# Performance work log

Measured on AMD Instinct MI355X. Metric: run time of the kernel, lower is better.

## Reference

```python
import jax, jax.numpy as jnp
import numpy as np

N_NODES, N_EDGES, N_FEAT = 50000, 500000, 128
HID, LAT, N_GRAPHS = 256, 64, 512
HEADS, DH = 8, 32  # GAT: 8 heads x 32 = 256
EPS = 1e-5


def _seg_softmax(logits, seg, num):
    m = jax.ops.segment_max(logits, seg, num_segments=num)
    m = jnp.where(jnp.isfinite(m), m, 0.0)
    e = jnp.exp(logits - m[seg])
    s = jax.ops.segment_sum(e, seg, num_segments=num)
    return e / jnp.maximum(s[seg], 1e-16)


def _bn(h, g, b):  # BatchNorm1d, batch statistics
    mu = h.mean(0)
    var = h.var(0)
    return (h - mu) * jax.lax.rsqrt(var + EPS) * g + b


def _ln(h, g, b):
    mu = h.mean(-1, keepdims=True)
    var = h.var(-1, keepdims=True)
    return (h - mu) * jax.lax.rsqrt(var + EPS) * g + b


def setup_inputs() -> dict:
    key = jax.random.key(0)
    ks = iter(jax.random.split(key, 40))
    f = lambda *s: jax.random.normal(next(ks), s, dtype=jnp.float32) * 0.05
    inp = {
        'x': jax.random.normal(next(ks), (N_NODES, N_FEAT), dtype=jnp.float32),
        'W_emb': f(N_FEAT, HID), 'b_emb': f(HID),
        'W_gcn': f(HID, HID), 'b_gcn': f(HID),
        'W_gat': f(HID, HID), 'a_src': f(HEADS, DH), 'a_dst': f(HEADS, DH), 'b_gat': f(HID),
        'W_l': f(HID, HID), 'b_l': f(HID), 'W_r': f(HID, HID),
        'bn_gamma': jnp.ones((3, HID), jnp.float32), 'bn_beta': jnp.zeros((3, HID), jnp.float32),
        'Wg1': f(HID, HID // 2), 'bg1': f(HID // 2), 'Wg2': f(HID // 2, 1), 'bg2': f(1),
        'Wm1': f(HID, HID), 'bm1': f(HID), 'ln_m_g': jnp.ones(HID, jnp.float32), 'ln_m_b': jnp.zeros(HID, jnp.float32),
        'Wm2': f(HID, LAT), 'bm2': f(LAT),
        'Wv1': f(HID, HID), 'bv1': f(HID), 'ln_v_g': jnp.ones(HID, jnp.float32), 'ln_v_b': jnp.zeros(HID, jnp.float32),
        'Wv2': f(HID, LAT), 'bv2': f(LAT),
        'edge_index': jax.random.randint(next(ks), (2, N_EDGES), 0, N_NODES, dtype=jnp.int64),
        'batch': jnp.sort(jax.random.randint(next(ks), (N_NODES,), 0, N_GRAPHS, dtype=jnp.int64)),
    }
    return inp


def _forward(x, W_emb, b_emb, W_gcn, b_gcn, W_gat, a_src, a_dst, b_gat,
             W_l, b_l, W_r, bn_gamma, bn_beta, Wg1, bg1, Wg2, bg2,
             Wm1, bm1, ln_m_g, ln_m_b, Wm2, bm2, Wv1, bv1, ln_v_g, ln_v_b, Wv2, bv2,
             edge_index, batch):
    N = x.shape[0]
    loops = jnp.arange(N)
    src_sl = jnp.concatenate([edge_index[0], loops])  # with self-loops (GCN/GAT)
    dst_sl = jnp.concatenate([edge_index[1], loops])

    h = x @ W_emb + b_emb  # [N, HID]

    # --- layer 0: GCNConv ---
    deg = jax.ops.segment_sum(jnp.ones_like(dst_sl, dtype=h.dtype), dst_sl, num_segments=N)
    dis = jax.lax.rsqrt(deg)
    norm = dis[src_sl] * dis[dst_sl]  # [E+N]
    xt = h @ W_gcn
    out = jax.ops.segment_sum(xt[src_sl] * norm[:, None], dst_sl, num_segments=N) + b_gcn
    out = jax.nn.relu(_bn(out, bn_gamma[0], bn_beta[0]))
    h = h + out

    # --- layer 1: GATConv (8 heads, concat) ---
    xt = (h @ W_gat).reshape(N, HEADS, DH)
    al_src = (xt * a_src).sum(-1)  # [N, H]
    al_dst = (xt * a_dst).sum(-1)
    logits = jax.nn.leaky_relu(al_src[src_sl] + al_dst[dst_sl], 0.2)  # [E+N, H]
    alpha = _seg_softmax(logits, dst_sl, N)
    out = jax.ops.segment_sum(xt[src_sl] * alpha[:, :, None], dst_sl, num_segments=N)
    out = out.reshape(N, HID) + b_gat
    out = jax.nn.relu(_bn(out, bn_gamma[1], bn_beta[1]))
    h = h + out

    # --- layer 2: SAGEConv (mean aggregation, no self-loops) ---
    src, dst = edge_index[0], edge_index[1]
    cnt = jax.ops.segment_sum(jnp.ones_like(dst, dtype=h.dtype), dst, num_segments=N)
    nb_mean = jax.ops.segment_sum(h[src], dst, num_segments=N) / jnp.maximum(cnt, 1.0)[:, None]
    out = nb_mean @ W_l + b_l + h @ W_r
    out = jax.nn.relu(_bn(out, bn_gamma[2], bn_beta[2]))
    h = h + out

    # --- GlobalAttention pooling ---
    gate = (jax.nn.relu(h @ Wg1 + bg1) @ Wg2 + bg2)[:, 0]  # [N]
    w = _seg_softmax(gate, batch, N_GRAPHS)
    h_graph = jax.ops.segment_sum(h * w[:, None], batch, num_segments=N_GRAPHS)  # [G, HID]

    mu = jax.nn.relu(_ln(h_graph @ Wm1 + bm1, ln_m_g, ln_m_b)) @ Wm2 + bm2
    logvar = jax.nn.relu(_ln(h_graph @ Wv1 + bv1, ln_v_g, ln_v_b)) @ Wv2 + bv2
    return mu, logvar


def reference(x, W_emb, b_emb, W_gcn, b_gcn, W_gat, a_src, a_dst, b_gat,
              W_l, b_l, W_r, bn_gamma, bn_beta, Wg1, bg1, Wg2, bg2,
              Wm1, bm1, ln_m_g, ln_m_b, Wm2, bm2, Wv1, bv1, ln_v_g, ln_v_b, Wv2, bv2,
              edge_index, batch):
    return _forward(x, W_emb, b_emb, W_gcn, b_gcn, W_gat, a_src, a_dst, b_gat,
                    W_l, b_l, W_r, bn_gamma, bn_beta, Wg1, bg1, Wg2, bg2,
                    Wm1, bm1, ln_m_g, ln_m_b, Wm2, bm2, Wv1, bv1, ln_v_g, ln_v_b, Wv2, bv2,
                    edge_index, batch)
```

## Files before the change

kernel.cpp:

```cpp
#include <hip/hip_runtime.h>
#include <cstdint>
#include <cstddef>

#define N_NODES 50000
#define N_EDGES 500000
#define NG 512
#define HID 256
#define EPS 1e-5f
#define SCB 49

typedef __attribute__((ext_vector_type(8))) __bf16 bf16x8;
typedef __attribute__((ext_vector_type(8))) ushort u16x8;
typedef __attribute__((ext_vector_type(4))) float f32x4;

__device__ __forceinline__ ushort f2bf(float f) {
  uint32_t u = __float_as_uint(f);
  uint32_t r = (u + 0x7fffu + ((u >> 16) & 1u)) >> 16;
  return (ushort)r;
}
__device__ __forceinline__ float bfu(ushort u) { return __uint_as_float(((uint32_t)u) << 16); }
__device__ __forceinline__ float4 bf4(ushort4 u) {
  return make_float4(bfu(u.x), bfu(u.y), bfu(u.z), bfu(u.w));
}

__global__ void k_csr_count(const int* __restrict__ ei, int* __restrict__ cnt) {
  int e = blockIdx.x * 256 + threadIdx.x;
  if (e < N_EDGES) atomicAdd(&cnt[ei[N_EDGES + e]], 1);
}

__global__ void k_scan_part(const int* __restrict__ cnt, int* __restrict__ psum) {
  __shared__ int red[256];
  int tid = threadIdx.x;
  int i0 = blockIdx.x * 1024 + tid * 4;
  int s = 0;
  if (i0 + 4 <= N_NODES) {
    int4 v = *reinterpret_cast<const int4*>(cnt + i0);
    s = v.x + v.y + v.z + v.w;
  } else {
    for (int k = 0; k < 4; k++)
      if (i0 + k < N_NODES) s += cnt[i0 + k];
  }
  red[tid] = s;
  __syncthreads();
  for (int o = 128; o > 0; o >>= 1) {
    if (tid < o) red[tid] += red[tid + o];
    __syncthreads();
  }
  if (tid == 0) psum[blockIdx.x] = red[0];
}

__global__ void k_scan_top(const int* __restrict__ psum, int* __restrict__ boff,
                           int* __restrict__ row_ptr) {
  int t = threadIdx.x;
  int v = (t < SCB) ? psum[t] : 0;
  int own = v;
  for (int o = 1; o < 64; o <<= 1) {
    int u = __shfl_up(v, o);
    if (t >= o) v += u;
  }
  if (t < SCB) boff[t] = v - own;
  if (t == 63) row_ptr[N_NODES] = v;
}

__global__ void k_scan_out(const int* __restrict__ cnt, const int* __restrict__ boff,
                           int* __restrict__ row_ptr, float* __restrict__ dis) {
  __shared__ int ps[256];
  int tid = threadIdx.x;
  int i0 = blockIdx.x * 1024 + tid * 4;
  int v[4];
#pragma unroll
  for (int k = 0; k < 4; k++) v[k] = (i0 + k < N_NODES) ? cnt[i0 + k] : 0;
  int s = v[0] + v[1] + v[2] + v[3];
  ps[tid] = s;
  __syncthreads();
  for (int o = 1; o < 256; o <<= 1) {
    int add = (tid >= o) ? ps[tid - o] : 0;
    __syncthreads();
    ps[tid] += add;
    __syncthreads();
  }
  int run = boff[blockIdx.x] + ((tid > 0) ? ps[tid - 1] : 0);
#pragma unroll
  for (int k = 0; k < 4; k++) {
    if (i0 + k < N_NODES) {
      row_ptr[i0 + k] = run;
      dis[i0 + k] = rsqrtf((float)v[k] + 1.0f);
      run += v[k];
    }
  }
}

__global__ void k_csr_fill(const int* __restrict__ ei, const int* __restrict__ row_ptr,
                           int* __restrict__ fill, int* __restrict__ col_src) {
  int e = blockIdx.x * 256 + threadIdx.x;
  if (e >= N_EDGES) return;
  int s = ei[e], d = ei[N_EDGES + e];
  int pos = row_ptr[d] + atomicAdd(&fill[d], 1);
  col_src[pos] = s;
}

struct WtArgs {
  const float* src[6];
  ushort* dst[6];
  int K[6];
  int C[6];
  int off[6];
};

__global__ void k_wt_all(WtArgs a) {
  int b = blockIdx.x;
  int ji = 0;
#pragma unroll
  for (int t = 1; t < 6; t++)
    if (b >= a.off[t]) ji = t;
  int K = a.K[ji], C = a.C[ji];
  int i = (b - a.off[ji]) * 256 + threadIdx.x;
  int c = i / K, k = i - c * K;
  a.dst[ji][i] = f2bf(a.src[ji][k * C + c]);
}

template <int K, int C, bool DUAL, bool AFP32, bool GATE, bool GATAL>
__global__ __launch_bounds__(512) void k_mgemm(
    const void* __restrict__ A1v, const ushort* __restrict__ W1t,
    const ushort* __restrict__ A2, const ushort* __restrict__ W2t,
    const float* __restrict__ bias, ushort* __restrict__ out_bf,
    const float* __restrict__ gw, const float* __restrict__ gb,
    float* __restrict__ gate, const float* __restrict__ asv,
    const float* __restrict__ adv, float* __restrict__ als,
    float* __restrict__ ald, int M, int relu) {
  constexpr int KS = K / 32;
  constexpr int CHK = K / 8;
  constexpr int NPAN = C / 64;
  constexpr int NISS = (64 * CHK) / 512;
  constexpr int NTOT = NPAN * (DUAL ? 2 : 1);
  constexpr int PELEM = 64 * K;
  __shared__ ushort wlds[2 * PELEM];
  const int tid = threadIdx.x;
  const int lane = tid & 63;
  const int wid = tid >> 6;
  const int r16 = lane & 15;
  const int kg = lane >> 4;
  const int rbase = blockIdx.x * 128 + wid * 16;

  int arow = rbase + r16;
  if (arow >= M) arow = M - 1;

  bf16x8 af[KS], af2[KS];
  if constexpr (AFP32) {
    const float* ap = (const float*)A1v + (size_t)arow * K + kg * 8;
#pragma unroll
    for (int ks = 0; ks < KS; ks++) {
      float4 lo = *reinterpret_cast<const float4*>(ap + ks * 32);
      float4 hi = *reinterpret_cast<const float4*>(ap + ks * 32 + 4);
      union { u16x8 u; bf16x8 b; } cv;
      cv.u = (u16x8){f2bf(lo.x), f2bf(lo.y), f2bf(lo.z), f2bf(lo.w),
                     f2bf(hi.x), f2bf(hi.y), f2bf(hi.z), f2bf(hi.w)};
      af[ks] = cv.b;
    }
  } else {
    const ushort* ap = (const ushort*)A1v + (size_t)arow * K + kg * 8;
#pragma unroll
    for (int ks = 0; ks < KS; ks++)
      af[ks] = *reinterpret_cast<const bf16x8*>(ap + ks * 32);
  }
  if constexpr (DUAL) {
    const ushort* ap = A2 + (size_t)arow * K + kg * 8;
#pragma unroll
    for (int ks = 0; ks < KS; ks++)
      af2[ks] = *reinterpret_cast<const bf16x8*>(ap + ks * 32);
  }

  float greg[4] = {0.f, 0.f, 0.f, 0.f};
  f32x4 acc[4];

#define STAGE_ASYNC(WSRC, PAN, BUF)                                            \
  {                                                                            \
    const ushort* base_ = (WSRC) + (size_t)((PAN) * 64) * K;                   \
    _Pragma("unroll") for (int j = 0; j < NISS; j++) {                         \
      int p_ = j * 512 + tid;                                                  \
      int c_ = p_ / CHK, jj_ = p_ % CHK;                                       \
      const ushort* g_ = base_ + c_ * K + (jj_ ^ (c_ & 7)) * 8;                \
      ushort* l_ = &wlds[(BUF) * PELEM + (j * 512 + wid * 64) * 8];            \
      __builtin_amdgcn_global_load_lds(                                        \
          (const __attribute__((address_space(1))) void*)(g_),                 \
          (__attribute__((address_space(3))) void*)(l_), 16, 0, 0);            \
    }                                                                          \
  }

#define COMPUTE(AF, BUF)                                                       \
  {                                                                            \
    const ushort* wb_ = &wlds[(BUF) * PELEM];                                  \
    _Pragma("unroll") for (int ct = 0; ct < 4; ct++) {                         \
      bf16x8 wf[KS];                                                           \
      int colr = ct * 16 + r16;                                                \
      _Pragma("unroll") for (int ks = 0; ks < KS; ks++) {                      \
        int slot = colr * CHK + ((ks * 4 + kg) ^ (r16 & 7));                   \
        wf[ks] = *reinterpret_cast<const bf16x8*>(&wb_[slot * 8]);             \
      }                                                                        \
      _Pragma("unroll") for (int ks = 0; ks < KS; ks++)                        \
        acc[ct] = __builtin_amdgcn_mfma_f32_16x16x32_bf16((AF)[ks], wf[ks],    \
                                                          acc[ct], 0, 0, 0);   \
    }                                                                          \
  }

  STAGE_ASYNC(W1t, 0, 0);
  __syncthreads();

#pragma unroll
  for (int q = 0; q < NTOT; q++) {
    const int pan = DUAL ? (q >> 1) : q;
    const int pass = DUAL ? (q & 1) : 0;
    const int cur = q & 1;
    const int c0 = pan * 64;
    if (pass == 0) {
#pragma unroll
      for (int ct = 0; ct < 4; ct++) acc[ct] = (f32x4){0.f, 0.f, 0.f, 0.f};
    }
    if (q + 1 < NTOT) {
      const int npan = DUAL ? ((q + 1) >> 1) : (q + 1);
      const ushort* Wq = (DUAL && ((q + 1) & 1)) ? W2t : W1t;
      STAGE_ASYNC(Wq, npan, cur ^ 1);
    }
    if (DUAL && pass) {
      COMPUTE(af2, cur);
    } else {
      COMPUTE(af, cur);
    }
    if (pass == (DUAL ? 1 : 0)) {
      if constexpr (GATE) {
#pragma unroll
        for (int ct = 0; ct < 4; ct++) {
          int col = c0 + ct * 16 + r16;
          float bv = bias[col];
          float wv = gw[col];
#pragma unroll
          for (int i = 0; i < 4; i++) {
            float v = fmaxf(acc[ct][i] + bv, 0.f);
            greg[i] = fmaf(v, wv, greg[i]);
          }
        }
      } else {
#pragma unroll
        for (int ct = 0; ct < 4; ct++) {
          int col = c0 + ct * 16 + r16;
          float bv = bias ? bias[col] : 0.f;
#pragma unroll
          for (int i = 0; i < 4; i++) {
            int row = rbase + kg * 4 + i;
            if (row < M) {
              float v = acc[ct][i] + bv;
              if (relu) v = fmaxf(v, 0.f);
              out_bf[(size_t)row * C + col] = f2bf(v);
            }
          }
        }
      }
      if constexpr (GATAL) {
        float ps_[2][4], pd_[2][4];
#pragma unroll
        for (int h2 = 0; h2 < 2; h2++)
#pragma unroll
          for (int i = 0; i < 4; i++) { ps_[h2][i] = 0.f; pd_[h2][i] = 0.f; }
#pragma unroll
        for (int ct = 0; ct < 4; ct++) {
          int col = c0 + ct * 16 + r16;
          float as_ = asv[col], ad_ = adv[col];
          int h2 = ct >> 1;
#pragma unroll
          for (int i = 0; i < 4; i++) {
            ps_[h2][i] = fmaf(acc[ct][i], as_, ps_[h2][i]);
            pd_[h2][i] = fmaf(acc[ct][i], ad_, pd_[h2][i]);
          }
        }
#pragma unroll
        for (int h2 = 0; h2 < 2; h2++)
#pragma unroll
          for (int i = 0; i < 4; i++) {
#pragma unroll
            for (int o = 1; o < 16; o <<= 1) {
              ps_[h2][i] += __shfl_xor(ps_[h2][i], o);
              pd_[h2][i] += __shfl_xor(pd_[h2][i], o);
            }
          }
        if (r16 == 0) {
#pragma unroll
          for (int i = 0; i < 4; i++) {
            int row = rbase + kg * 4 + i;
            if (row < M) {
              als[row * 8 + pan * 2 + 0] = ps_[0][i];
              ald[row * 8 + pan * 2 + 0] = pd_[0][i];
              als[row * 8 + pan * 2 + 1] = ps_[1][i];
              ald[row * 8 + pan * 2 + 1] = pd_[1][i];
            }
          }
        }
      }
    }
    __syncthreads();
  }

  if constexpr (GATE) {
#pragma unroll
    for (int i = 0; i < 4; i++) {
#pragma unroll
      for (int o = 1; o < 16; o <<= 1) greg[i] += __shfl_xor(greg[i], o);
    }
    if (r16 == 0) {
      float b0 = gb[0];
#pragma unroll
      for (int i = 0; i < 4; i++) {
        int row = rbase + kg * 4 + i;
        if (row < M) gate[row] = greg[i] + b0;
      }
    }
  }
#undef STAGE_ASYNC
#undef COMPUTE
}

__global__ void k_gcn_agg(const ushort* __restrict__ xt, const float* __restrict__ dis,
                          const int* __restrict__ row_ptr, const int* __restrict__ col_src,
                          const float* __restrict__ b_gcn, ushort* __restrict__ outb) {
  int node = blockIdx.x * 4 + (threadIdx.x >> 6);
  if (node >= N_NODES) return;
  int lane = threadIdx.x & 63;
  int half = lane >> 5;
  int c0 = (lane & 31) * 8;
  float di = dis[node];
  float acc[8];
#pragma unroll
  for (int j = 0; j < 8; j++) acc[j] = 0.f;
  int b = row_ptr[node], e = row_ptr[node + 1];
  int g0 = b;
  for (; g0 + 8 <= e; g0 += 8) {
    int i0 = g0 + half * 4;
    int s0 = col_src[i0], s1 = col_src[i0 + 1], s2 = col_src[i0 + 2], s3 = col_src[i0 + 3];
    float w0 = di * dis[s0], w1 = di * dis[s1], w2 = di * dis[s2], w3 = di * dis[s3];
    u16x8 u0 = *reinterpret_cast<const u16x8*>(xt + (size_t)s0 * HID + c0);
    u16x8 u1 = *reinterpret_cast<const u16x8*>(xt + (size_t)s1 * HID + c0);
    u16x8 u2 = *reinterpret_cast<const u16x8*>(xt + (size_t)s2 * HID + c0);
    u16x8 u3 = *reinterpret_cast<const u16x8*>(xt + (size_t)s3 * HID + c0);
#pragma unroll
    for (int j = 0; j < 8; j++) {
      acc[j] = fmaf(bfu(u0[j]), w0, acc[j]);
      acc[j] = fmaf(bfu(u1[j]), w1, acc[j]);
      acc[j] = fmaf(bfu(u2[j]), w2, acc[j]);
      acc[j] = fmaf(bfu(u3[j]), w3, acc[j]);
    }
  }
  for (; g0 + 4 <= e; g0 += 4) {
    int i0 = g0 + half * 2;
    int s0 = col_src[i0], s1 = col_src[i0 + 1];
    float w0 = di * dis[s0], w1 = di * dis[s1];
    u16x8 u0 = *reinterpret_cast<const u16x8*>(xt + (size_t)s0 * HID + c0);
    u16x8 u1 = *reinterpret_cast<const u16x8*>(xt + (size_t)s1 * HID + c0);
#pragma unroll
    for (int j = 0; j < 8; j++) {
      acc[j] = fmaf(bfu(u0[j]), w0, acc[j]);
      acc[j] = fmaf(bfu(u1[j]), w1, acc[j]);
    }
  }
  {
    int i0 = g0 + half * 2;
    int s0 = 0, s1 = 0;
    float w0 = 0.f, w1 = 0.f;
    if (i0 < e) { s0 = col_src[i0]; w0 = di * dis[s0]; }
    if (i0 + 1 < e) { s1 = col_src[i0 + 1]; w1 = di * dis[s1]; }
    u16x8 u0 = *reinterpret_cast<const u16x8*>(xt + (size_t)s0 * HID + c0);
    u16x8 u1 = *reinterpret_cast<const u16x8*>(xt + (size_t)s1 * HID + c0);
#pragma unroll
    for (int j = 0; j < 8; j++) {
      acc[j] = fmaf(bfu(u0[j]), w0, acc[j]);
      acc[j] = fmaf(bfu(u1[j]), w1, acc[j]);
    }
  }
#pragma unroll
  for (int j = 0; j < 8; j++) acc[j] += __shfl_xor(acc[j], 32);
  if (!half) {
    u16x8 un = *reinterpret_cast<const u16x8*>(xt + (size_t)node * HID + c0);
    float w0 = di * di;
    u16x8 r;
#pragma unroll
    for (int j = 0; j < 8; j++) {
      float v = fmaf(bfu(un[j]), w0, acc[j]) + b_gcn[c0 + j];
      r[j] = f2bf(v);
    }
    *reinterpret_cast<u16x8*>(outb + (size_t)node * HID + c0) = r;
  }
}

__device__ __forceinline__ float leaky02(float x) { return x > 0.f ? x : 0.2f * x; }

__global__ void k_gat_agg(const ushort* __restrict__ xt, const float* __restrict__ alsrc,
                          const float* __restrict__ aldst, const int* __restrict__ row_ptr,
                          const int* __restrict__ col_src, const float* __restrict__ b_gat,
                          ushort* __restrict__ outb) {
  int node = blockIdx.x * 4 + (threadIdx.x >> 6);
  if (node >= N_NODES) return;
  int lane = threadIdx.x & 63;
  int half = lane >> 5;
  int l32 = lane & 31;
  int c0 = l32 * 8;
  int hh = l32 >> 2;
  float ad = aldst[node * 8 + hh];
  float acc[8];
#pragma unroll
  for (int j = 0; j < 8; j++) acc[j] = 0.f;
  float s = 0.f;
  int b = row_ptr[node], e = row_ptr[node + 1];
  int g0 = b;
  for (; g0 + 8 <= e; g0 += 8) {
    int i0 = g0 + half * 4;
    int s0 = col_src[i0], s1 = col_src[i0 + 1], s2 = col_src[i0 + 2], s3 = col_src[i0 + 3];
    float g0v = alsrc[s0 * 8 + hh], g1v = alsrc[s1 * 8 + hh];
    float g2v = alsrc[s2 * 8 + hh], g3v = alsrc[s3 * 8 + hh];
    u16x8 u0 = *reinterpret_cast<const u16x8*>(xt + (size_t)s0 * HID + c0);
    u16x8 u1 = *reinterpret_cast<const u16x8*>(xt + (size_t)s1 * HID + c0);
    u16x8 u2 = *reinterpret_cast<const u16x8*>(xt + (size_t)s2 * HID + c0);
    u16x8 u3 = *reinterpret_cast<const u16x8*>(xt + (size_t)s3 * HID + c0);
    float a0 = __expf(leaky02(g0v + ad));
    float a1 = __expf(leaky02(g1v + ad));
    float a2 = __expf(leaky02(g2v + ad));
    float a3 = __expf(leaky02(g3v + ad));
    s += a0 + a1 + a2 + a3;
#pragma unroll
    for (int j = 0; j < 8; j++) {
      acc[j] = fmaf(bfu(u0[j]), a0, acc[j]);
      acc[j] = fmaf(bfu(u1[j]), a1, acc[j]);
      acc[j] = fmaf(bfu(u2[j]), a2, acc[j]);
      acc[j] = fmaf(bfu(u3[j]), a3, acc[j]);
    }
  }
  for (; g0 + 4 <= e; g0 += 4) {
    int i0 = g0 + half * 2;
    int s0 = col_src[i0], s1 = col_src[i0 + 1];
    float a0 = __expf(leaky02(alsrc[s0 * 8 + hh] + ad));
    float a1 = __expf(leaky02(alsrc[s1 * 8 + hh] + ad));
    u16x8 u0 = *reinterpret_cast<const u16x8*>(xt + (size_t)s0 * HID + c0);
    u16x8 u1 = *reinterpret_cast<const u16x8*>(xt + (size_t)s1 * HID + c0);
    s += a0 + a1;
#pragma unroll
    for (int j = 0; j < 8; j++) {
      acc[j] = fmaf(bfu(u0[j]), a0, acc[j]);
      acc[j] = fmaf(bfu(u1[j]), a1, acc[j]);
    }
  }
  {
    int i0 = g0 + half * 2;
    int s0 = 0, s1 = 0;
    float a0 = 0.f, a1 = 0.f;
    if (i0 < e) { s0 = col_src[i0]; a0 = __expf(leaky02(alsrc[s0 * 8 + hh] + ad)); }
    if (i0 + 1 < e) { s1 = col_src[i0 + 1]; a1 = __expf(leaky02(alsrc[s1 * 8 + hh] + ad)); }
    u16x8 u0 = *reinterpret_cast<const u16x8*>(xt + (size_t)s0 * HID + c0);
    u16x8 u1 = *reinterpret_cast<const u16x8*>(xt + (size_t)s1 * HID + c0);
    s += a0 + a1;
#pragma unroll
    for (int j = 0; j < 8; j++) {
      acc[j] = fmaf(bfu(u0[j]), a0, acc[j]);
      acc[j] = fmaf(bfu(u1[j]), a1, acc[j]);
    }
  }
#pragma unroll
  for (int j = 0; j < 8; j++) acc[j] += __shfl_xor(acc[j], 32);
  s += __shfl_xor(s, 32);
  if (!half) {
    float e0 = __expf(leaky02(alsrc[node * 8 + hh] + ad));
    u16x8 un = *reinterpret_cast<const u16x8*>(xt + (size_t)node * HID + c0);
    float inv_s = 1.0f / (s + e0);
    u16x8 r;
#pragma unroll
    for (int j = 0; j < 8; j++) {
      float v = fmaf(bfu(un[j]), e0, acc[j]) * inv_s + b_gat[c0 + j];
      r[j] = f2bf(v);
    }
    *reinterpret_cast<u16x8*>(outb + (size_t)node * HID + c0) = r;
  }
}

__global__ void k_sage_agg(const ushort* __restrict__ h, const int* __restrict__ row_ptr,
                           const int* __restrict__ col_src, ushort* __restrict__ outb) {
  int node = blockIdx.x * 4 + (threadIdx.x >> 6);
  if (node >= N_NODES) return;
  int lane = threadIdx.x & 63;
  int half = lane >> 5;
  int c0 = (lane & 31) * 8;
  float acc[8];
#pragma unroll
  for (int j = 0; j < 8; j++) acc[j] = 0.f;
  int b = row_ptr[node], e = row_ptr[node + 1];
  int g0 = b;
  for (; g0 + 8 <= e; g0 += 8) {
    int i0 = g0 + half * 4;
    int s0 = col_src[i0], s1 = col_src[i0 + 1], s2 = col_src[i0 + 2], s3 = col_src[i0 + 3];
    u16x8 u0 = *reinterpret_cast<const u16x8*>(h + (size_t)s0 * HID + c0);
    u16x8 u1 = *reinterpret_cast<const u16x8*>(h + (size_t)s1 * HID + c0);
    u16x8 u2 = *reinterpret_cast<const u16x8*>(h + (size_t)s2 * HID + c0);
    u16x8 u3 = *reinterpret_cast<const u16x8*>(h + (size_t)s3 * HID + c0);
#pragma unroll
    for (int j = 0; j < 8; j++)
      acc[j] += (bfu(u0[j]) + bfu(u1[j])) + (bfu(u2[j]) + bfu(u3[j]));
  }
  for (; g0 + 4 <= e; g0 += 4) {
    int i0 = g0 + half * 2;
    int s0 = col_src[i0], s1 = col_src[i0 + 1];
    u16x8 u0 = *reinterpret_cast<const u16x8*>(h + (size_t)s0 * HID + c0);
    u16x8 u1 = *reinterpret_cast<const u16x8*>(h + (size_t)s1 * HID + c0);
#pragma unroll
    for (int j = 0; j < 8; j++) acc[j] += bfu(u0[j]) + bfu(u1[j]);
  }
  {
    int i0 = g0 + half * 2;
    int s0 = 0, s1 = 0;
    float w0 = 0.f, w1 = 0.f;
    if (i0 < e) { s0 = col_src[i0]; w0 = 1.f; }
    if (i0 + 1 < e) { s1 = col_src[i0 + 1]; w1 = 1.f; }
    u16x8 u0 = *reinterpret_cast<const u16x8*>(h + (size_t)s0 * HID + c0);
    u16x8 u1 = *reinterpret_cast<const u16x8*>(h + (size_t)s1 * HID + c0);
#pragma unroll
    for (int j = 0; j < 8; j++) {
      acc[j] = fmaf(bfu(u0[j]), w0, acc[j]);
      acc[j] = fmaf(bfu(u1[j]), w1, acc[j]);
    }
  }
#pragma unroll
  for (int j = 0; j < 8; j++) acc[j] += __shfl_xor(acc[j], 32);
  if (!half) {
    float inv = 1.0f / fmaxf((float)(e - b), 1.0f);
    u16x8 r;
#pragma unroll
    for (int j = 0; j < 8; j++) r[j] = f2bf(acc[j] * inv);
    *reinterpret_cast<u16x8*>(outb + (size_t)node * HID + c0) = r;
  }
}

__global__ void k_bn_stats(const ushort* __restrict__ x, float* __restrict__ stats) {
  int c = threadIdx.x;
  float s = 0.f, q = 0.f;
  for (int r = blockIdx.x; r < N_NODES; r += gridDim.x) {
    float v = bfu(x[(size_t)r * HID + c]);
    s += v;
    q = fmaf(v, v, q);
  }
  atomicAdd(&stats[c], s);
  atomicAdd(&stats[HID + c], q);
}

__global__ void k_bn_apply(const ushort* __restrict__ x, const float* __restrict__ stats,
                           const float* __restrict__ gamma, const float* __restrict__ beta,
                           ushort* __restrict__ h_bf) {
  const float invN = 1.0f / (float)N_NODES;
  int total = N_NODES * 64;
  for (int i = blockIdx.x * 256 + threadIdx.x; i < total; i += gridDim.x * 256) {
    int c4 = (i & 63) * 4;
    float4 xv = bf4(*reinterpret_cast<const ushort4*>(x + (size_t)i * 4));
    float4 sm = *reinterpret_cast<const float4*>(stats + c4);
    float4 sq = *reinterpret_cast<const float4*>(stats + HID + c4);
    float4 gm = *reinterpret_cast<const float4*>(gamma + c4);
    float4 bt = *reinterpret_cast<const float4*>(beta + c4);
    float4 hv = bf4(*reinterpret_cast<const ushort4*>(h_bf + (size_t)i * 4));
#define BN1(f)                                                    \
  {                                                               \
    float mu = sm.f * invN;                                       \
    float var = sq.f * invN - mu * mu;                            \
    float sc = gm.f * rsqrtf(var + EPS);                          \
    float v = (xv.f - mu) * sc + bt.f;                            \
    hv.f += fmaxf(v, 0.f);                                        \
  }
    BN1(x) BN1(y) BN1(z) BN1(w)
#undef BN1
    *reinterpret_cast<ushort4*>(h_bf + (size_t)i * 4) =
        make_ushort4(f2bf(hv.x), f2bf(hv.y), f2bf(hv.z), f2bf(hv.w));
  }
}

__global__ void k_gstart(const int* __restrict__ batch, int* __restrict__ gstart) {
  int g = blockIdx.x * 256 + threadIdx.x;
  if (g > NG) return;
  int lo = 0, hi = N_NODES;
  while (lo < hi) {
    int mid = (lo + hi) >> 1;
    if (batch[mid] < g) lo = mid + 1; else hi = mid;
  }
  gstart[g] = lo;
}

__global__ void k_pool(const ushort* __restrict__ hb, const float* __restrict__ gate,
                       const int* __restrict__ gstart, float* __restrict__ hg) {
  __shared__ float red[256];
  __shared__ float wbuf[256];
  int g = blockIdx.x, tid = threadIdx.x;
  int b = gstart[g], e = gstart[g + 1];
  float m = -1e30f;
  for (int r = b + tid; r < e; r += 256) m = fmaxf(m, gate[r]);
  red[tid] = m;
  __syncthreads();
  for (int o = 128; o > 0; o >>= 1) {
    if (tid < o) red[tid] = fmaxf(red[tid], red[tid + o]);
    __syncthreads();
  }
  m = red[0];
  __syncthreads();
  float s = 0.f;
  for (int r = b + tid; r < e; r += 256) s += __expf(gate[r] - m);
  red[tid] = s;
  __syncthreads();
  for (int o = 128; o > 0; o >>= 1) {
    if (tid < o) red[tid] += red[tid + o];
    __syncthreads();
  }
  float inv = 1.0f / fmaxf(red[0], 1e-16f);
  __syncthreads();
  float acc = 0.f;
  for (int cb = b; cb < e; cb += 256) {
    int r = cb + tid;
    wbuf[tid] = (r < e) ? __expf(gate[r] - m) : 0.f;
    __syncthreads();
    int n = min(256, e - cb);
    for (int j = 0; j < n; j++)
      acc = fmaf(bfu(hb[(size_t)(cb + j) * HID + tid]), wbuf[j], acc);
    __syncthreads();
  }
  hg[(size_t)g * HID + tid] = acc * inv;
}

__global__ void k_mlp(const float* __restrict__ hg, const float* __restrict__ W1,
                      const float* __restrict__ b1, const float* __restrict__ lng,
                      const float* __restrict__ lnb, const float* __restrict__ W2,
                      const float* __restrict__ b2, float* __restrict__ out) {
  __shared__ float row[HID];
  __shared__ float z[HID];
  __shared__ float red[HID];
  int g = blockIdx.x, tid = threadIdx.x;
  row[tid] = hg[(size_t)g * HID + tid];
  __syncthreads();
  float acc = b1[tid];
  for (int k = 0; k < HID; k++) acc = fmaf(row[k], W1[(size_t)k * HID + tid], acc);
  red[tid] = acc;
  __syncthreads();
  for (int o = 128; o > 0; o >>= 1) {
    if (tid < o) red[tid] += red[tid + o];
    __syncthreads();
  }
  float mu = red[0] * (1.0f / HID);
  __syncthreads();
  red[tid] = acc * acc;
  __syncthreads();
  for (int o = 128; o > 0; o >>= 1) {
    if (tid < o) red[tid] += red[tid + o];
    __syncthreads();
  }
  float var = red[0] * (1.0f / HID) - mu * mu;
  float zz = (acc - mu) * rsqrtf(var + EPS) * lng[tid] + lnb[tid];
  z[tid] = fmaxf(zz, 0.f);
  __syncthreads();
  if (tid < 64) {
    float o = b2[tid];
    for (int k = 0; k < HID; k++) o = fmaf(z[k], W2[(size_t)k * 64 + tid], o);
    out[(size_t)g * 64 + tid] = o;
  }
}

extern "C" void kernel_launch(void* const* d_in, const int* in_sizes, int n_in,
                              void* d_out, int out_size, void* d_ws, size_t ws_size,
                              hipStream_t stream) {
  const float* x     = (const float*)d_in[0];
  const float* W_emb = (const float*)d_in[1];
  const float* b_emb = (const float*)d_in[2];
  const float* W_gcn = (const float*)d_in[3];
  const float* b_gcn = (const float*)d_in[4];
  const float* W_gat = (const float*)d_in[5];
  const float* a_src = (const float*)d_in[6];
  const float* a_dst = (const float*)d_in[7];
  const float* b_gat = (const float*)d_in[8];
  const float* W_l   = (const float*)d_in[9];
  const float* b_l   = (const float*)d_in[10];
  const float* W_r   = (const float*)d_in[11];
  const float* bn_g  = (const float*)d_in[12];
  const float* bn_b  = (const float*)d_in[13];
  const float* Wg1   = (const float*)d_in[14];
  const float* bg1   = (const float*)d_in[15];
  const float* Wg2   = (const float*)d_in[16];
  const float* bg2   = (const float*)d_in[17];
  const float* Wm1   = (const float*)d_in[18];
  const float* bm1   = (const float*)d_in[19];
  const float* lnmg  = (const float*)d_in[20];
  const float* lnmb  = (const float*)d_in[21];
  const float* Wm2   = (const float*)d_in[22];
  const float* bm2   = (const float*)d_in[23];
  const float* Wv1   = (const float*)d_in[24];
  const float* bv1   = (const float*)d_in[25];
  const float* lnvg  = (const float*)d_in[26];
  const float* lnvb  = (const float*)d_in[27];
  const float* Wv2   = (const float*)d_in[28];
  const float* bv2   = (const float*)d_in[29];
  const int* ei      = (const int*)d_in[30];
  const int* batch   = (const int*)d_in[31];
  float* out = (float*)d_out;

  float* ws = (float*)d_ws;
  float* h     = ws;
  float* t1    = h + (size_t)N_NODES * HID;
  float* alsrc = t1 + (size_t)N_NODES * HID;
  float* aldst = alsrc + N_NODES * 8;
  float* dis   = aldst + N_NODES * 8;
  float* gate  = dis + N_NODES;
  float* hg    = gate + N_NODES;
  float* zbase = hg + NG * HID;
  float* bnst  = zbase;
  int* row_cnt = (int*)(zbase + 3 * 512);
  int* fill    = row_cnt + N_NODES;
  int* row_ptr = fill + N_NODES;
  int* col_src = row_ptr + N_NODES + 1;
  int* gstart  = col_src + N_EDGES;
  int* psum    = gstart + NG + 1;
  int* boff    = psum + 64;

  ushort* t1b = (ushort*)t1;

  size_t off = (size_t)((char*)(boff + 64) - (char*)d_ws);
  off = (off + 15) & ~(size_t)15;
  ushort* h_bf   = (ushort*)((char*)d_ws + off);
  ushort* t0_bf  = h_bf + (size_t)N_NODES * HID;
  ushort* wemb_t = t0_bf + (size_t)N_NODES * HID;
  ushort* wgcn_t = wemb_t + 128 * 256;
  ushort* wgat_t = wgcn_t + 256 * 256;
  ushort* wr_t   = wgat_t + 256 * 256;
  ushort* wl_t   = wr_t + 256 * 256;
  ushort* wg1_t  = wl_t + 256 * 256;

  size_t zbytes = (size_t)3 * 512 * 4 + 2 * (size_t)N_NODES * 4;
  hipMemsetAsync(zbase, 0, zbytes, stream);

  k_csr_count<<<(N_EDGES + 255) / 256, 256, 0, stream>>>(ei, row_cnt);
  k_scan_part<<<SCB, 256, 0, stream>>>(row_cnt, psum);
  k_scan_top<<<1, 64, 0, stream>>>(psum, boff, row_ptr);
  k_scan_out<<<SCB, 256, 0, stream>>>(row_cnt, boff, row_ptr, dis);
  k_csr_fill<<<(N_EDGES + 255) / 256, 256, 0, stream>>>(ei, row_ptr, fill, col_src);

  WtArgs wa;
  wa.src[0] = W_emb; wa.dst[0] = wemb_t; wa.K[0] = 128; wa.C[0] = 256; wa.off[0] = 0;
  wa.src[1] = W_gcn; wa.dst[1] = wgcn_t; wa.K[1] = 256; wa.C[1] = 256; wa.off[1] = 128;
  wa.src[2] = W_gat; wa.dst[2] = wgat_t; wa.K[2] = 256; wa.C[2] = 256; wa.off[2] = 384;
  wa.src[3] = W_r;   wa.dst[3] = wr_t;   wa.K[3] = 256; wa.C[3] = 256; wa.off[3] = 640;
  wa.src[4] = W_l;   wa.dst[4] = wl_t;   wa.K[4] = 256; wa.C[4] = 256; wa.off[4] = 896;
  wa.src[5] = Wg1;   wa.dst[5] = wg1_t;  wa.K[5] = 256; wa.C[5] = 128; wa.off[5] = 1152;
  k_wt_all<<<1280, 256, 0, stream>>>(wa);

  const int RB = (N_NODES + 127) / 128;
  const int AB = (N_NODES + 3) / 4;

  k_mgemm<128, 256, false, true, false, false><<<RB, 512, 0, stream>>>(
      x, wemb_t, nullptr, nullptr, b_emb, h_bf, nullptr, nullptr, nullptr,
      nullptr, nullptr, nullptr, nullptr, N_NODES, 0);

  k_mgemm<256, 256, false, false, false, false><<<RB, 512, 0, stream>>>(
      h_bf, wgcn_t, nullptr, nullptr, nullptr, t0_bf, nullptr, nullptr, nullptr,
      nullptr, nullptr, nullptr, nullptr, N_NODES, 0);
  k_gcn_agg<<<AB, 256, 0, stream>>>(t0_bf, dis, row_ptr, col_src, b_gcn, t1b);
  k_bn_stats<<<256, 256, 0, stream>>>(t1b, bnst);
  k_bn_apply<<<1024, 256, 0, stream>>>(t1b, bnst, bn_g, bn_b, h_bf);

  k_mgemm<256, 256, false, false, false, true><<<RB, 512, 0, stream>>>(
      h_bf, wgat_t, nullptr, nullptr, nullptr, t0_bf, nullptr, nullptr, nullptr,
      a_src, a_dst, alsrc, aldst, N_NODES, 0);
  k_gat_agg<<<AB, 256, 0, stream>>>(t0_bf, alsrc, aldst, row_ptr, col_src, b_gat, t1b);
  k_bn_stats<<<256, 256, 0, stream>>>(t1b, bnst + 512);
  k_bn_apply<<<1024, 256, 0, stream>>>(t1b, bnst + 512, bn_g + HID, bn_b + HID, h_bf);

  k_sage_agg<<<AB, 256, 0, stream>>>(h_bf, row_ptr, col_src, t0_bf);
  k_mgemm<256, 256, true, false, false, false><<<RB, 512, 0, stream>>>(
      h_bf, wr_t, t0_bf, wl_t, b_l, t1b, nullptr, nullptr, nullptr,
      nullptr, nullptr, nullptr, nullptr, N_NODES, 0);
  k_bn_stats<<<256, 256, 0, stream>>>(t1b, bnst + 1024);
  k_bn_apply<<<1024, 256, 0, stream>>>(t1b, bnst + 1024, bn_g + 2 * HID, bn_b + 2 * HID, h_bf);

  k_mgemm<256, 128, false, false, true, false><<<RB, 512, 0, stream>>>(
      h_bf, wg1_t, nullptr, nullptr, bg1, nullptr, Wg2, bg2, gate,
      nullptr, nullptr, nullptr, nullptr, N_NODES, 1);
  k_gstart<<<3, 256, 0, stream>>>(batch, gstart);
  k_pool<<<NG, 256, 0, stream>>>(h_bf, gate, gstart, hg);

  k_mlp<<<NG, 256, 0, stream>>>(hg, Wm1, bm1, lnmg, lnmb, Wm2, bm2, out);
  k_mlp<<<NG, 256, 0, stream>>>(hg, Wv1, bv1, lnvg, lnvb, Wv2, bv2, out + (size_t)NG * 64);
}
```

Measured before the change: 604.5 us.

## Fuse BatchNorm apply into following GEMM A-load and vectorize BN stats

BatchNorm statistics now use 8-wide vector loads with shared-memory reduction before the global atomics. Scale and shift are computed once per channel in a tiny coefficient kernel. For the GCN and SAGE layers, the normalize, ReLU and residual step is folded into the next GEMM's A-operand load, which also writes the updated residual back. This removes two standalone apply passes over the 50000x256 activation. The GAT layer keeps a simpler apply kernel.

Result: faster. 549.4 us (-9.1%).

```diff
diff --git a/kernel.cpp b/kernel.cpp
--- a/kernel.cpp
+++ b/kernel.cpp
@@ -119,7 +119,7 @@
   a.dst[ji][i] = f2bf(a.src[ji][k * C + c]);
 }
 
-template <int K, int C, bool DUAL, bool AFP32, bool GATE, bool GATAL>
+template <int K, int C, bool DUAL, bool AFP32, bool GATE, bool GATAL, bool BNF>
 __global__ __launch_bounds__(512) void k_mgemm(
     const void* __restrict__ A1v, const ushort* __restrict__ W1t,
     const ushort* __restrict__ A2, const ushort* __restrict__ W2t,
@@ -127,7 +127,8 @@
     const float* __restrict__ gw, const float* __restrict__ gb,
     float* __restrict__ gate, const float* __restrict__ asv,
     const float* __restrict__ adv, float* __restrict__ als,
-    float* __restrict__ ald, int M, int relu) {
+    float* __restrict__ ald, const float* __restrict__ scsh,
+    ushort* __restrict__ hbuf, int M, int relu) {
   constexpr int KS = K / 32;
   constexpr int CHK = K / 8;
   constexpr int NPAN = C / 64;
@@ -142,11 +143,36 @@
   const int kg = lane >> 4;
   const int rbase = blockIdx.x * 128 + wid * 16;
 
+  const bool avalid = (rbase + r16) < M;
   int arow = rbase + r16;
   if (arow >= M) arow = M - 1;
 
   bf16x8 af[KS], af2[KS];
-  if constexpr (AFP32) {
+  if constexpr (BNF) {
+    const ushort* xp = (const ushort*)A1v + (size_t)arow * K + kg * 8;
+    ushort* hp = hbuf + (size_t)arow * K + kg * 8;
+#pragma unroll
+    for (int ks = 0; ks < KS; ks++) {
+      int col = kg * 8 + ks * 32;
+      u16x8 xv = *reinterpret_cast<const u16x8*>(xp + ks * 32);
+      u16x8 hv = *reinterpret_cast<const u16x8*>(hp + ks * 32);
+      float4 sc0 = *reinterpret_cast<const float4*>(scsh + col);
+      float4 sc1 = *reinterpret_cast<const float4*>(scsh + col + 4);
+      float4 sh0 = *reinterpret_cast<const float4*>(scsh + 256 + col);
+      float4 sh1 = *reinterpret_cast<const float4*>(scsh + 256 + col + 4);
+      float scv[8] = {sc0.x, sc0.y, sc0.z, sc0.w, sc1.x, sc1.y, sc1.z, sc1.w};
+      float shv[8] = {sh0.x, sh0.y, sh0.z, sh0.w, sh1.x, sh1.y, sh1.z, sh1.w};
+      union { u16x8 u; bf16x8 b; } cv;
+#pragma unroll
+      for (int j = 0; j < 8; j++) {
+        float v = fmaf(bfu(xv[j]), scv[j], shv[j]);
+        float hn = bfu(hv[j]) + fmaxf(v, 0.f);
+        cv.u[j] = f2bf(hn);
+      }
+      af[ks] = cv.b;
+      if (avalid) *reinterpret_cast<u16x8*>(hp + ks * 32) = cv.u;
+    }
+  } else if constexpr (AFP32) {
     const float* ap = (const float*)A1v + (size_t)arow * K + kg * 8;
 #pragma unroll
     for (int ks = 0; ks < KS; ks++) {
@@ -533,41 +559,62 @@
   }
 }
 
-__global__ void k_bn_stats(const ushort* __restrict__ x, float* __restrict__ stats) {
+__global__ __launch_bounds__(256) void k_bn_stats(const ushort* __restrict__ x,
+                                                  float* __restrict__ stats) {
+  int tid = threadIdx.x;
+  int cg = tid & 31;
+  int rs = tid >> 5;
+  int c0 = cg * 8;
+  float s[8], q[8];
+#pragma unroll
+  for (int j = 0; j < 8; j++) { s[j] = 0.f; q[j] = 0.f; }
+  for (int r = blockIdx.x * 8 + rs; r < N_NODES; r += gridDim.x * 8) {
+    u16x8 v = *reinterpret_cast<const u16x8*>(x + (size_t)r * HID + c0);
+#pragma unroll
+    for (int j = 0; j < 8; j++) {
+      float f = bfu(v[j]);
+      s[j] += f;
+      q[j] = fmaf(f, f, q[j]);
+    }
+  }
+  __shared__ float ls[512];
+  ls[tid] = 0.f;
+  ls[tid + 256] = 0.f;
+  __syncthreads();
+#pragma unroll
+  for (int j = 0; j < 8; j++) {
+    atomicAdd(&ls[c0 + j], s[j]);
+    atomicAdd(&ls[256 + c0 + j], q[j]);
+  }
+  __syncthreads();
+  atomicAdd(&stats[tid], ls[tid]);
+  atomicAdd(&stats[tid + 256], ls[tid + 256]);
+}
+
+__global__ void k_bn_coef(const float* __restrict__ stats, const float* __restrict__ gamma,
+                          const float* __restrict__ beta, float* __restrict__ scsh) {
   int c = threadIdx.x;
-  float s = 0.f, q = 0.f;
-  for (int r = blockIdx.x; r < N_NODES; r += gridDim.x) {
-    float v = bfu(x[(size_t)r * HID + c]);
-    s += v;
-    q = fmaf(v, v, q);
-  }
-  atomicAdd(&stats[c], s);
-  atomicAdd(&stats[HID + c], q);
-}
-
-__global__ void k_bn_apply(const ushort* __restrict__ x, const float* __restrict__ stats,
-                           const float* __restrict__ gamma, const float* __restrict__ beta,
+  const float invN = 1.0f / (float)N_NODES;
+  float mu = stats[c] * invN;
+  float var = stats[256 + c] * invN - mu * mu;
+  float sc = gamma[c] * rsqrtf(var + EPS);
+  scsh[c] = sc;
+  scsh[256 + c] = beta[c] - mu * sc;
+}
+
+__global__ void k_bn_apply(const ushort* __restrict__ x, const float* __restrict__ scsh,
                            ushort* __restrict__ h_bf) {
-  const float invN = 1.0f / (float)N_NODES;
   int total = N_NODES * 64;
   for (int i = blockIdx.x * 256 + threadIdx.x; i < total; i += gridDim.x * 256) {
     int c4 = (i & 63) * 4;
     float4 xv = bf4(*reinterpret_cast<const ushort4*>(x + (size_t)i * 4));
-    float4 sm = *reinterpret_cast<const float4*>(stats + c4);
-    float4 sq = *reinterpret_cast<const float4*>(stats + HID + c4);
-    float4 gm = *reinterpret_cast<const float4*>(gamma + c4);
-    float4 bt = *reinterpret_cast<const float4*>(beta + c4);
+    float4 sc = *reinterpret_cast<const float4*>(scsh + c4);
+    float4 sh = *reinterpret_cast<const float4*>(scsh + 256 + c4);
     float4 hv = bf4(*reinterpret_cast<const ushort4*>(h_bf + (size_t)i * 4));
-#define BN1(f)                                                    \
-  {                                                               \
-    float mu = sm.f * invN;                                       \
-    float var = sq.f * invN - mu * mu;                            \
-    float sc = gm.f * rsqrtf(var + EPS);                          \
-    float v = (xv.f - mu) * sc + bt.f;                            \
-    hv.f += fmaxf(v, 0.f);                                        \
-  }
-    BN1(x) BN1(y) BN1(z) BN1(w)
-#undef BN1
+    hv.x += fmaxf(fmaf(xv.x, sc.x, sh.x), 0.f);
+    hv.y += fmaxf(fmaf(xv.y, sc.y, sh.y), 0.f);
+    hv.z += fmaxf(fmaf(xv.z, sc.z, sh.z), 0.f);
+    hv.w += fmaxf(fmaf(xv.w, sc.w, sh.w), 0.f);
     *reinterpret_cast<ushort4*>(h_bf + (size_t)i * 4) =
         make_ushort4(f2bf(hv.x), f2bf(hv.y), f2bf(hv.z), f2bf(hv.w));
   }
@@ -714,10 +761,11 @@
   int* gstart  = col_src + N_EDGES;
   int* psum    = gstart + NG + 1;
   int* boff    = psum + 64;
+  float* scsh  = (float*)(boff + 64);
 
   ushort* t1b = (ushort*)t1;
 
-  size_t off = (size_t)((char*)(boff + 64) - (char*)d_ws);
+  size_t off = (size_t)((char*)(scsh + 3 * 512) - (char*)d_ws);
   off = (off + 15) & ~(size_t)15;
   ushort* h_bf   = (ushort*)((char*)d_ws + off);
   ushort* t0_bf  = h_bf + (size_t)N_NODES * HID;
@@ -749,34 +797,35 @@
   const int RB = (N_NODES + 127) / 128;
   const int AB = (N_NODES + 3) / 4;
 
-  k_mgemm<128, 256, false, true, false, false><<<RB, 512, 0, stream>>>(
+  k_mgemm<128, 256, false, true, false, false, false><<<RB, 512, 0, stream>>>(
       x, wemb_t, nullptr, nullptr, b_emb, h_bf, nullptr, nullptr, nullptr,
-      nullptr, nullptr, nullptr, nullptr, N_NODES, 0);
-
-  k_mgemm<256, 256, false, false, false, false><<<RB, 512, 0, stream>>>(
+      nullptr, nullptr, nullptr, nullptr, nullptr, nullptr, N_NODES, 0);
+
+  k_mgemm<256, 256, false, false, false, false, false><<<RB, 512, 0, stream>>>(
       h_bf, wgcn_t, nullptr, nullptr, nullptr, t0_bf, nullptr, nullptr, nullptr,
-      nullptr, nullptr, nullptr, nullptr, N_NODES, 0);
+      nullptr, nullptr, nullptr, nullptr, nullptr, nullptr, N_NODES, 0);
   k_gcn_agg<<<AB, 256, 0, stream>>>(t0_bf, dis, row_ptr, col_src, b_gcn, t1b);
-  k_bn_stats<<<256, 256, 0, stream>>>(t1b, bnst);
-  k_bn_apply<<<1024, 256, 0, stream>>>(t1b, bnst, bn_g, bn_b, h_bf);
-
-  k_mgemm<256, 256, false, false, false, true><<<RB, 512, 0, stream>>>(
-      h_bf, wgat_t, nullptr, nullptr, nullptr, t0_bf, nullptr, nullptr, nullptr,
-      a_src, a_dst, alsrc, aldst, N_NODES, 0);
+  k_bn_stats<<<1024, 256, 0, stream>>>(t1b, bnst);
+  k_bn_coef<<<1, 256, 0, stream>>>(bnst, bn_g, bn_b, scsh);
+
+  k_mgemm<256, 256, false, false, false, true, true><<<RB, 512, 0, stream>>>(
+      t1b, wgat_t, nullptr, nullptr, nullptr, t0_bf, nullptr, nullptr, nullptr,
+      a_src, a_dst, alsrc, aldst, scsh, h_bf, N_NODES, 0);
   k_gat_agg<<<AB, 256, 0, stream>>>(t0_bf, alsrc, aldst, row_ptr, col_src, b_gat, t1b);
-  k_bn_stats<<<256, 256, 0, stream>>>(t1b, bnst + 512);
-  k_bn_apply<<<1024, 256, 0, stream>>>(t1b, bnst + 512, bn_g + HID, bn_b + HID, h_bf);
+  k_bn_stats<<<1024, 256, 0, stream>>>(t1b, bnst + 512);
+  k_bn_coef<<<1, 256, 0, stream>>>(bnst + 512, bn_g + HID, bn_b + HID, scsh + 512);
+  k_bn_apply<<<1024, 256, 0, stream>>>(t1b, scsh + 512, h_bf);
 
   k_sage_agg<<<AB, 256, 0, stream>>>(h_bf, row_ptr, col_src, t0_bf);
-  k_mgemm<256, 256, true, false, false, false><<<RB, 512, 0, stream>>>(
+  k_mgemm<256, 256, true, false, false, false, false><<<RB, 512, 0, stream>>>(
       h_bf, wr_t, t0_bf, wl_t, b_l, t1b, nullptr, nullptr, nullptr,
-      nullptr, nullptr, nullptr, nullptr, N_NODES, 0);
-  k_bn_stats<<<256, 256, 0, stream>>>(t1b, bnst + 1024);
-  k_bn_apply<<<1024, 256, 0, stream>>>(t1b, bnst + 1024, bn_g + 2 * HID, bn_b + 2 * HID, h_bf);
-
-  k_mgemm<256, 128, false, false, true, false><<<RB, 512, 0, stream>>>(
-      h_bf, wg1_t, nullptr, nullptr, bg1, nullptr, Wg2, bg2, gate,
-      nullptr, nullptr, nullptr, nullptr, N_NODES, 1);
+      nullptr, nullptr, nullptr, nullptr, nullptr, nullptr, N_NODES, 0);
+  k_bn_stats<<<1024, 256, 0, stream>>>(t1b, bnst + 1024);
+  k_bn_coef<<<1, 256, 0, stream>>>(bnst + 1024, bn_g + 2 * HID, bn_b + 2 * HID, scsh + 1024);
+
+  k_mgemm<256, 128, false, false, true, false, true><<<RB, 512, 0, stream>>>(
+      t1b, wg1_t, nullptr, nullptr, bg1, nullptr, Wg2, bg2, gate,
+      nullptr, nullptr, nullptr, nullptr, scsh + 1024, h_bf, N_NODES, 1);
   k_gstart<<<3, 256, 0, stream>>>(batch, gstart);
   k_pool<<<NG, 256, 0, stream>>>(h_bf, gate, gstart, hg);
 
```
